# Kernel tuning notes

Hardware: AMD Instinct MI355X
Metric: run time of the kernel (lower is better)

The kernel has to match this reference:

```python
import jax, jax.numpy as jnp
import numpy as np

T, B, H, L = 2048, 4096, 4, 3

def setup_inputs() -> dict:
    key = jax.random.key(0)
    ks = jax.random.split(key, 6)
    scale = 1.0 / np.sqrt(H)  # PyTorch nn.RNN init range ~U(-1/sqrt(H), 1/sqrt(H)); use normal*scale for simplicity
    return {
        "x": jax.random.normal(ks[0], (T, B, H), dtype=jnp.float32),
        "h": jax.random.normal(ks[1], (L, B, H), dtype=jnp.float32),
        "Wih": jax.random.normal(ks[2], (L, H, H), dtype=jnp.float32) * scale,
        "Whh": jax.random.normal(ks[3], (L, H, H), dtype=jnp.float32) * scale,
        "bih": jax.random.normal(ks[4], (L, H), dtype=jnp.float32) * scale,
        "bhh": jax.random.normal(ks[5], (L, H), dtype=jnp.float32) * scale,
    }

def _rnn_layer(x, h0, W_ih, W_hh, b_ih, b_hh):
    # x: (T, B, H); h0: (B, H). Vanilla tanh RNN, matching torch nn.RNN layer math:
    # h_t = tanh(x_t @ W_ih^T + b_ih + h_{t-1} @ W_hh^T + b_hh)
    b = b_ih + b_hh
    def step(h, xt):
        h_new = jnp.tanh(xt @ W_ih.T + h @ W_hh.T + b)
        return h_new, h_new
    _, ys = jax.lax.scan(step, h0, x)
    return ys  # (T, B, H)

def reference(x, h, Wih, Whh, bih, bhh):
    out = x
    for l in range(Wih.shape[0]):  # small fixed layer count (3)
        out = _rnn_layer(out, h[l], Wih[l], Whh[l], bih[l], bhh[l])
    return out  # (T, B, H): all-timestep outputs of last layer
```

## Files before the change

kernel.cpp:

```cpp
#include <hip/hip_runtime.h>

#define TSTEPS 2048
#define BATCH  4096
#define HID    4
#define STRIDE (BATCH*HID)
#define CH     32
#define NCHUNK (TSTEPS/CH)
#define NPH    69

#define QB(v,k) __int_as_float(__builtin_amdgcn_update_dpp( \
    0, __float_as_int(v), (k)*0x55, 0xF, 0xF, true))

__device__ __forceinline__ float fast_exp2(float x) {
#if __has_builtin(__builtin_amdgcn_exp2f)
  return __builtin_amdgcn_exp2f(x);
#else
  return exp2f(x);
#endif
}
__device__ __forceinline__ float fast_rcp(float x) {
#if __has_builtin(__builtin_amdgcn_rcpf)
  return __builtin_amdgcn_rcpf(x);
#else
  return 1.0f / x;
#endif
}

__device__ __forceinline__ void xload(float* ldst, const float* gsrc) {
  __builtin_amdgcn_global_load_lds(
      (const __attribute__((address_space(1))) void*)gsrc,
      (__attribute__((address_space(3))) void*)ldst, 4, 0, 0);
}

__global__ __launch_bounds__(256) void rnn_pipe4(
    const float* __restrict__ X,
    const float* __restrict__ H0,
    const float* __restrict__ Wih,
    const float* __restrict__ Whh,
    const float* __restrict__ bih,
    const float* __restrict__ bhh,
    float* __restrict__ Y)
{
  const int lane = threadIdx.x & 63;
  const int wid  = threadIdx.x >> 6;
  const int g    = blockIdx.x * 64 + lane;
  const int j    = g & 3;
  const float K  = 2.8853900817779268f;

  __shared__ float iface[3][2][CH/2][64][2];
  __shared__ float xbuf[3][CH][64];

  float whp[HID], wip[HID], cbn = 0.0f, r = 0.0f;
  {
    const int Lt = wid - 1;
    const int Ln = wid;
    if (wid >= 1) {
#pragma unroll
      for (int k = 0; k < HID; ++k)
        whp[k] = -2.0f * K * Whh[(Lt*HID + j)*HID + k];
      r = 0.5f * (1.0f - H0[Lt*STRIDE + g]);
    }
    if (wid == 0) {
      float wsum = 0.0f;
#pragma unroll
      for (int k = 0; k < HID; ++k) {
        wip[k] = K * Wih[(Ln*HID + j)*HID + k];
        wsum  += Whh[(Ln*HID + j)*HID + k];
      }
      cbn = K * (bih[Ln*HID + j] + bhh[Ln*HID + j] + wsum);
    } else if (wid <= 2) {
      float wsum = 0.0f;
#pragma unroll
      for (int k = 0; k < HID; ++k) {
        float wik = Wih[(Ln*HID + j)*HID + k];
        wip[k] = -2.0f * K * wik;
        wsum  += Whh[(Ln*HID + j)*HID + k] + wik;
      }
      cbn = K * (bih[Ln*HID + j] + bhh[Ln*HID + j] + wsum);
    }
  }

  const float* __restrict__ xp = X + g;

  if (wid == 0) {
    __builtin_amdgcn_sched_barrier(0);
    asm volatile("s_waitcnt vmcnt(0)" ::: "memory");
#pragma unroll
    for (int u = 0; u < CH; ++u)
      xload(&xbuf[0][u][0], xp + (size_t)(0*CH + u) * STRIDE);
#pragma unroll
    for (int u = 0; u < CH; ++u)
      xload(&xbuf[1][u][0], xp + (size_t)(1*CH + u) * STRIDE);
  }

  auto phase = [&](int p, int slot) {
    if (wid == 0) {
      if (p <= NCHUNK - 1) {
        const int par = p & 1;
        asm volatile("s_waitcnt vmcnt(32)" ::: "memory");
        __builtin_amdgcn_sched_barrier(0);
        float xv[CH];
#pragma unroll
        for (int u = 0; u < CH; ++u) xv[u] = xbuf[slot][u][lane];
        __builtin_amdgcn_sched_barrier(0);
        float apend = 0.0f;
#pragma unroll
        for (int u = 0; u < CH; ++u) {
          float a = cbn;
          a = fmaf(QB(xv[u], 0), wip[0], a);
          a = fmaf(QB(xv[u], 1), wip[1], a);
          a = fmaf(QB(xv[u], 2), wip[2], a);
          a = fmaf(QB(xv[u], 3), wip[3], a);
          if (u & 1) {
            float2 pr = {apend, a};
            *(float2*)&iface[0][par][u >> 1][lane][0] = pr;
          } else {
            apend = a;
          }
        }
#pragma unroll
        for (int u = 0; u < CH; ++u) {
          int tn = (p + 2) * CH + u;
          if (tn > TSTEPS - 1) tn = TSTEPS - 1;
          xload(&xbuf[(slot+2)%3][u][0], xp + (size_t)tn * STRIDE);
        }
      }
    } else {
      const int m = p - wid;
      if (m >= 0 && m <= NCHUNK - 1) {
        const int par = m & 1;
        float av[CH];
#pragma unroll
        for (int p2 = 0; p2 < CH/2; ++p2) {
          float2 v = *(const float2*)&iface[wid-1][par][p2][lane][0];
          av[2*p2]   = v.x;
          av[2*p2+1] = v.y;
        }
        __builtin_amdgcn_sched_barrier(0);
        if (wid <= 2) {
          float apend = 0.0f;
#pragma unroll
          for (int u = 0; u < CH; ++u) {
            float d0 = QB(r, 0), d1 = QB(r, 1), d2 = QB(r, 2), d3 = QB(r, 3);
            if (u > 0) {
              float a = cbn;
              a = fmaf(d0, wip[0], a);
              a = fmaf(d1, wip[1], a);
              a = fmaf(d2, wip[2], a);
              a = fmaf(d3, wip[3], a);
              if (u & 1) {
                apend = a;
              } else {
                float2 pr = {apend, a};
                *(float2*)&iface[wid][par][(u-2) >> 1][lane][0] = pr;
              }
            }
            float t0 = fmaf(d0, whp[0], av[u]);
            float t1 = d1 * whp[1];
            t0 = fmaf(d2, whp[2], t0);
            t1 = fmaf(d3, whp[3], t1);
            r = fast_rcp(fast_exp2(t0 + t1) + 1.0f);
          }
          {
            float d0 = QB(r, 0), d1 = QB(r, 1), d2 = QB(r, 2), d3 = QB(r, 3);
            float a = cbn;
            a = fmaf(d0, wip[0], a);
            a = fmaf(d1, wip[1], a);
            a = fmaf(d2, wip[2], a);
            a = fmaf(d3, wip[3], a);
            float2 pr = {apend, a};
            *(float2*)&iface[wid][par][(CH-2) >> 1][lane][0] = pr;
          }
        } else {
          const int base = m * CH;
#pragma unroll
          for (int u = 0; u < CH; ++u) {
            float t0 = fmaf(QB(r, 0), whp[0], av[u]);
            float t1 =      QB(r, 1) * whp[1];
            t0 = fmaf(QB(r, 2), whp[2], t0);
            t1 = fmaf(QB(r, 3), whp[3], t1);
            r = fast_rcp(fast_exp2(t0 + t1) + 1.0f);
            Y[(size_t)(base + u) * STRIDE + g] = fmaf(-2.0f, r, 1.0f);
          }
        }
      }
    }

    __builtin_amdgcn_sched_barrier(0);
    asm volatile("s_waitcnt lgkmcnt(0)" ::: "memory");
    __builtin_amdgcn_s_barrier();
    __builtin_amdgcn_sched_barrier(0);
  };

  for (int p = 0; p < NPH; p += 3) {
    phase(p + 0, 0);
    phase(p + 1, 1);
    phase(p + 2, 2);
  }

  if (wid == 0) asm volatile("s_waitcnt vmcnt(0)" ::: "memory");
}

extern "C" void kernel_launch(void* const* d_in, const int* in_sizes, int n_in,
                              void* d_out, int out_size, void* d_ws, size_t ws_size,
                              hipStream_t stream) {
  const float* X   = (const float*)d_in[0];
  const float* H0  = (const float*)d_in[1];
  const float* Wih = (const float*)d_in[2];
  const float* Whh = (const float*)d_in[3];
  const float* bih = (const float*)d_in[4];
  const float* bhh = (const float*)d_in[5];
  float* Y = (float*)d_out;

  rnn_pipe4<<<dim3(STRIDE / 64), dim3(256), 0, stream>>>(X, H0, Wih, Whh, bih, bhh, Y);
}
```

Before: 102.7 us.

## Interleave two independent recurrence chains per wave with dual producer waves

Each block now handles 128 columns instead of 64. Two producer waves load x and compute the layer-0 input projection, one per 64-column half. Each consumer wave advances two independent recurrence chains (A and B) in an interleaved way. The aim is to hide the latency of the serial dpp, exp and rcp dependency chain by giving the scheduler two independent chains. In exchange there are half as many blocks, 5 waves per block, more LDS per block and higher register pressure.

```diff
diff --git a/kernel.cpp b/kernel.cpp
--- a/kernel.cpp
+++ b/kernel.cpp
@@ -32,7 +32,7 @@
       (__attribute__((address_space(3))) void*)ldst, 4, 0, 0);
 }
 
-__global__ __launch_bounds__(256) void rnn_pipe4(
+__global__ __launch_bounds__(320) void rnn_dualp(
     const float* __restrict__ X,
     const float* __restrict__ H0,
     const float* __restrict__ Wih,
@@ -42,33 +42,36 @@
     float* __restrict__ Y)
 {
   const int lane = threadIdx.x & 63;
-  const int wid  = threadIdx.x >> 6;
-  const int g    = blockIdx.x * 64 + lane;
-  const int j    = g & 3;
+  const int w    = threadIdx.x >> 6;
+  const bool isP = (w == 0) || (w == 4);
+  const int  pg  = (w == 4) ? 1 : 0;
+  const int  gA  = blockIdx.x * 128 + lane;
+  const int  gB  = gA + 64;
+  const int  gP  = pg ? gB : gA;
+  const int  j   = lane & 3;
   const float K  = 2.8853900817779268f;
 
-  __shared__ float iface[3][2][CH/2][64][2];
-  __shared__ float xbuf[3][CH][64];
-
-  float whp[HID], wip[HID], cbn = 0.0f, r = 0.0f;
-  {
-    const int Lt = wid - 1;
-    const int Ln = wid;
-    if (wid >= 1) {
-#pragma unroll
-      for (int k = 0; k < HID; ++k)
-        whp[k] = -2.0f * K * Whh[(Lt*HID + j)*HID + k];
-      r = 0.5f * (1.0f - H0[Lt*STRIDE + g]);
+  __shared__ float xbuf[2][3][CH][64];
+  __shared__ float aif[3][2][2][CH/2][64][2];
+
+  float whp[HID], wip[HID], cbn = 0.0f, rA = 0.0f, rB = 0.0f;
+  if (isP) {
+    float wsum = 0.0f;
+#pragma unroll
+    for (int k = 0; k < HID; ++k) {
+      wip[k] = K * Wih[(0*HID + j)*HID + k];
+      wsum  += Whh[(0*HID + j)*HID + k];
     }
-    if (wid == 0) {
-      float wsum = 0.0f;
-#pragma unroll
-      for (int k = 0; k < HID; ++k) {
-        wip[k] = K * Wih[(Ln*HID + j)*HID + k];
-        wsum  += Whh[(Ln*HID + j)*HID + k];
-      }
-      cbn = K * (bih[Ln*HID + j] + bhh[Ln*HID + j] + wsum);
-    } else if (wid <= 2) {
+    cbn = K * (bih[0*HID + j] + bhh[0*HID + j] + wsum);
+  } else {
+    const int Lt = w - 1;
+#pragma unroll
+    for (int k = 0; k < HID; ++k)
+      whp[k] = -2.0f * K * Whh[(Lt*HID + j)*HID + k];
+    rA = 0.5f * (1.0f - H0[Lt*STRIDE + gA]);
+    rB = 0.5f * (1.0f - H0[Lt*STRIDE + gB]);
+    if (w <= 2) {
+      const int Ln = w;
       float wsum = 0.0f;
 #pragma unroll
       for (int k = 0; k < HID; ++k) {
@@ -80,28 +83,28 @@
     }
   }
 
-  const float* __restrict__ xp = X + g;
-
-  if (wid == 0) {
+  const float* __restrict__ xp = X + gP;
+
+  if (isP) {
     __builtin_amdgcn_sched_barrier(0);
     asm volatile("s_waitcnt vmcnt(0)" ::: "memory");
 #pragma unroll
     for (int u = 0; u < CH; ++u)
-      xload(&xbuf[0][u][0], xp + (size_t)(0*CH + u) * STRIDE);
+      xload(&xbuf[pg][0][u][0], xp + (size_t)(0*CH + u) * STRIDE);
 #pragma unroll
     for (int u = 0; u < CH; ++u)
-      xload(&xbuf[1][u][0], xp + (size_t)(1*CH + u) * STRIDE);
+      xload(&xbuf[pg][1][u][0], xp + (size_t)(1*CH + u) * STRIDE);
   }
 
   auto phase = [&](int p, int slot) {
-    if (wid == 0) {
+    if (isP) {
       if (p <= NCHUNK - 1) {
         const int par = p & 1;
         asm volatile("s_waitcnt vmcnt(32)" ::: "memory");
         __builtin_amdgcn_sched_barrier(0);
         float xv[CH];
 #pragma unroll
-        for (int u = 0; u < CH; ++u) xv[u] = xbuf[slot][u][lane];
+        for (int u = 0; u < CH; ++u) xv[u] = xbuf[pg][slot][u][lane];
         __builtin_amdgcn_sched_barrier(0);
         float apend = 0.0f;
 #pragma unroll
@@ -113,7 +116,7 @@
           a = fmaf(QB(xv[u], 3), wip[3], a);
           if (u & 1) {
             float2 pr = {apend, a};
-            *(float2*)&iface[0][par][u >> 1][lane][0] = pr;
+            *(float2*)&aif[0][pg][par][u >> 1][lane][0] = pr;
           } else {
             apend = a;
           }
@@ -122,65 +125,93 @@
         for (int u = 0; u < CH; ++u) {
           int tn = (p + 2) * CH + u;
           if (tn > TSTEPS - 1) tn = TSTEPS - 1;
-          xload(&xbuf[(slot+2)%3][u][0], xp + (size_t)tn * STRIDE);
+          xload(&xbuf[pg][(slot+2)%3][u][0], xp + (size_t)tn * STRIDE);
         }
       }
     } else {
-      const int m = p - wid;
+      const int m = p - w;
       if (m >= 0 && m <= NCHUNK - 1) {
         const int par = m & 1;
-        float av[CH];
-#pragma unroll
-        for (int p2 = 0; p2 < CH/2; ++p2) {
-          float2 v = *(const float2*)&iface[wid-1][par][p2][lane][0];
-          av[2*p2]   = v.x;
-          av[2*p2+1] = v.y;
+        float avA[CH], avB[CH];
+#pragma unroll
+        for (int q = 0; q < CH/2; ++q) {
+          float2 vA = *(const float2*)&aif[w-1][0][par][q][lane][0];
+          avA[2*q] = vA.x; avA[2*q+1] = vA.y;
+          float2 vB = *(const float2*)&aif[w-1][1][par][q][lane][0];
+          avB[2*q] = vB.x; avB[2*q+1] = vB.y;
         }
         __builtin_amdgcn_sched_barrier(0);
-        if (wid <= 2) {
-          float apend = 0.0f;
+        if (w <= 2) {
+          float apA = 0.0f, apB = 0.0f;
 #pragma unroll
           for (int u = 0; u < CH; ++u) {
-            float d0 = QB(r, 0), d1 = QB(r, 1), d2 = QB(r, 2), d3 = QB(r, 3);
+            float a0 = QB(rA, 0), a1 = QB(rA, 1), a2 = QB(rA, 2), a3 = QB(rA, 3);
+            float b0 = QB(rB, 0), b1 = QB(rB, 1), b2 = QB(rB, 2), b3 = QB(rB, 3);
             if (u > 0) {
-              float a = cbn;
-              a = fmaf(d0, wip[0], a);
-              a = fmaf(d1, wip[1], a);
-              a = fmaf(d2, wip[2], a);
-              a = fmaf(d3, wip[3], a);
+              float aa = cbn;
+              aa = fmaf(a0, wip[0], aa);
+              aa = fmaf(a1, wip[1], aa);
+              aa = fmaf(a2, wip[2], aa);
+              aa = fmaf(a3, wip[3], aa);
+              float ab = cbn;
+              ab = fmaf(b0, wip[0], ab);
+              ab = fmaf(b1, wip[1], ab);
+              ab = fmaf(b2, wip[2], ab);
+              ab = fmaf(b3, wip[3], ab);
               if (u & 1) {
-                apend = a;
+                apA = aa; apB = ab;
               } else {
-                float2 pr = {apend, a};
-                *(float2*)&iface[wid][par][(u-2) >> 1][lane][0] = pr;
+                float2 prA = {apA, aa};
+                *(float2*)&aif[w][0][par][(u-2) >> 1][lane][0] = prA;
+                float2 prB = {apB, ab};
+                *(float2*)&aif[w][1][par][(u-2) >> 1][lane][0] = prB;
               }
             }
-            float t0 = fmaf(d0, whp[0], av[u]);
-            float t1 = d1 * whp[1];
-            t0 = fmaf(d2, whp[2], t0);
-            t1 = fmaf(d3, whp[3], t1);
-            r = fast_rcp(fast_exp2(t0 + t1) + 1.0f);
+            float tA0 = fmaf(a0, whp[0], avA[u]);
+            float tA1 = a1 * whp[1];
+            tA0 = fmaf(a2, whp[2], tA0);
+            tA1 = fmaf(a3, whp[3], tA1);
+            rA = fast_rcp(fast_exp2(tA0 + tA1) + 1.0f);
+            float tB0 = fmaf(b0, whp[0], avB[u]);
+            float tB1 = b1 * whp[1];
+            tB0 = fmaf(b2, whp[2], tB0);
+            tB1 = fmaf(b3, whp[3], tB1);
+            rB = fast_rcp(fast_exp2(tB0 + tB1) + 1.0f);
           }
           {
-            float d0 = QB(r, 0), d1 = QB(r, 1), d2 = QB(r, 2), d3 = QB(r, 3);
-            float a = cbn;
-            a = fmaf(d0, wip[0], a);
-            a = fmaf(d1, wip[1], a);
-            a = fmaf(d2, wip[2], a);
-            a = fmaf(d3, wip[3], a);
-            float2 pr = {apend, a};
-            *(float2*)&iface[wid][par][(CH-2) >> 1][lane][0] = pr;
+            float a0 = QB(rA, 0), a1 = QB(rA, 1), a2 = QB(rA, 2), a3 = QB(rA, 3);
+            float b0 = QB(rB, 0), b1 = QB(rB, 1), b2 = QB(rB, 2), b3 = QB(rB, 3);
+            float aa = cbn;
+            aa = fmaf(a0, wip[0], aa);
+            aa = fmaf(a1, wip[1], aa);
+            aa = fmaf(a2, wip[2], aa);
+            aa = fmaf(a3, wip[3], aa);
+            float ab = cbn;
+            ab = fmaf(b0, wip[0], ab);
+            ab = fmaf(b1, wip[1], ab);
+            ab = fmaf(b2, wip[2], ab);
+            ab = fmaf(b3, wip[3], ab);
+            float2 prA = {apA, aa};
+            *(float2*)&aif[w][0][par][(CH-2) >> 1][lane][0] = prA;
+            float2 prB = {apB, ab};
+            *(float2*)&aif[w][1][par][(CH-2) >> 1][lane][0] = prB;
           }
         } else {
           const int base = m * CH;
 #pragma unroll
           for (int u = 0; u < CH; ++u) {
-            float t0 = fmaf(QB(r, 0), whp[0], av[u]);
-            float t1 =      QB(r, 1) * whp[1];
-            t0 = fmaf(QB(r, 2), whp[2], t0);
-            t1 = fmaf(QB(r, 3), whp[3], t1);
-            r = fast_rcp(fast_exp2(t0 + t1) + 1.0f);
-            Y[(size_t)(base + u) * STRIDE + g] = fmaf(-2.0f, r, 1.0f);
+            float tA0 = fmaf(QB(rA, 0), whp[0], avA[u]);
+            float tA1 =      QB(rA, 1) * whp[1];
+            tA0 = fmaf(QB(rA, 2), whp[2], tA0);
+            tA1 = fmaf(QB(rA, 3), whp[3], tA1);
+            rA = fast_rcp(fast_exp2(tA0 + tA1) + 1.0f);
+            float tB0 = fmaf(QB(rB, 0), whp[0], avB[u]);
+            float tB1 =      QB(rB, 1) * whp[1];
+            tB0 = fmaf(QB(rB, 2), whp[2], tB0);
+            tB1 = fmaf(QB(rB, 3), whp[3], tB1);
+            rB = fast_rcp(fast_exp2(tB0 + tB1) + 1.0f);
+            Y[(size_t)(base + u) * STRIDE + gA] = fmaf(-2.0f, rA, 1.0f);
+            Y[(size_t)(base + u) * STRIDE + gB] = fmaf(-2.0f, rB, 1.0f);
           }
         }
       }
@@ -198,7 +229,7 @@
     phase(p + 2, 2);
   }
 
-  if (wid == 0) asm volatile("s_waitcnt vmcnt(0)" ::: "memory");
+  if (isP) asm volatile("s_waitcnt vmcnt(0)" ::: "memory");
 }
 
 extern "C" void kernel_launch(void* const* d_in, const int* in_sizes, int n_in,
@@ -212,5 +243,5 @@
   const float* bhh = (const float*)d_in[5];
   float* Y = (float*)d_out;
 
-  rnn_pipe4<<<dim3(STRIDE / 64), dim3(256), 0, stream>>>(X, H0, Wih, Whh, bih, bhh, Y);
-}
+  rnn_dualp<<<dim3(STRIDE / 128), dim3(320), 0, stream>>>(X, H0, Wih, Whh, bih, bhh, Y);
+}
```

New measurement: 170.2 us. 65.8% more time.
